# Performance work log

Hardware: AMD Instinct MI355X
Metric: run time of the kernel (lower is better)

The kernel has to match this reference:

```python
import jax, jax.numpy as jnp
import numpy as np

HIDDEN = 4096
NUM_EXPERTS = 64
TOPK = 2
N_TOKENS = 16384


def setup_inputs() -> dict:
    key = jax.random.key(0)
    k_x, k_w, k_b = jax.random.split(key, 3)
    x = jax.random.normal(k_x, (N_TOKENS, HIDDEN), dtype=jnp.float32)
    # torch.nn.Linear: weight [out, in], bias [out], uniform(-1/sqrt(in), 1/sqrt(in))
    bound = 1.0 / np.sqrt(HIDDEN)
    W = jax.random.uniform(k_w, (NUM_EXPERTS, HIDDEN), dtype=jnp.float32, minval=-bound, maxval=bound)
    b = jax.random.uniform(k_b, (NUM_EXPERTS,), dtype=jnp.float32, minval=-bound, maxval=bound)
    return {"x": x, "W": W, "b": b}


def reference(x, W, b):
    # logits: [N, E] = x @ W.T + b
    logits = jnp.einsum("nh,eh->ne", x, W) + b
    probs = jax.nn.softmax(logits, axis=1)
    # torch.topk along dim=1 returns (values, indices), sorted descending
    values, indices = jax.lax.top_k(probs, TOPK)
    return values, indices
```

## Files before the change

### kernel.cpp

```cpp
#include <hip/hip_runtime.h>
#include <hip/hip_bf16.h>
#include <math.h>

#define HIDDEN   4096
#define NEXP     64
#define NTOK     16384
#define KCHUNKS  8
#define KC       (HIDDEN / KCHUNKS)
#define BK       32
#define BT       64
#define LDSS     68

__global__ __launch_bounds__(64, 2)
void gemm_partial(const float* __restrict__ x, const float* __restrict__ W,
                  float* __restrict__ part) {
    __shared__ float Xs[BK][LDSS];
    __shared__ float Ws[BK][LDSS];

    const int tid  = threadIdx.x;
    const int tile = blockIdx.x;
    const int kc   = blockIdx.y;
    const int t0   = tile * BT;

    const int lrow = tid & 7;
    const int lcol = tid >> 3;
    const int i    = tid & 7;
    const int j    = tid >> 3;

    float acc[8][8];
#pragma unroll
    for (int m = 0; m < 8; ++m)
#pragma unroll
        for (int e = 0; e < 8; ++e) acc[m][e] = 0.f;

    for (int kb = 0; kb < KC / BK; ++kb) {
        const int kg = kc * KC + kb * BK + lrow * 4;
#pragma unroll
        for (int p = 0; p < 8; ++p) {
            const int r = p * 8 + lcol;
            const float4 xv = *(const float4*)&x[(size_t)(t0 + r) * HIDDEN + kg];
            Xs[lrow * 4 + 0][r] = xv.x;
            Xs[lrow * 4 + 1][r] = xv.y;
            Xs[lrow * 4 + 2][r] = xv.z;
            Xs[lrow * 4 + 3][r] = xv.w;
            const float4 wv = *(const float4*)&W[(size_t)r * HIDDEN + kg];
            Ws[lrow * 4 + 0][r] = wv.x;
            Ws[lrow * 4 + 1][r] = wv.y;
            Ws[lrow * 4 + 2][r] = wv.z;
            Ws[lrow * 4 + 3][r] = wv.w;
        }
        __syncthreads();
#pragma unroll
        for (int kk = 0; kk < BK; ++kk) {
            const float4 xa = *(const float4*)&Xs[kk][i * 8];
            const float4 xb = *(const float4*)&Xs[kk][i * 8 + 4];
            const float4 wa = *(const float4*)&Ws[kk][j * 8];
            const float4 wb = *(const float4*)&Ws[kk][j * 8 + 4];
            const float xr[8] = {xa.x, xa.y, xa.z, xa.w, xb.x, xb.y, xb.z, xb.w};
            const float wr[8] = {wa.x, wa.y, wa.z, wa.w, wb.x, wb.y, wb.z, wb.w};
#pragma unroll
            for (int m = 0; m < 8; ++m)
#pragma unroll
                for (int e = 0; e < 8; ++e)
                    acc[m][e] = fmaf(xr[m], wr[e], acc[m][e]);
        }
        __syncthreads();
    }

    float* dst = part + ((size_t)kc * NTOK + t0) * NEXP;
#pragma unroll
    for (int m = 0; m < 8; ++m) {
        const int tok = i * 8 + m;
#pragma unroll
        for (int h = 0; h < 2; ++h) {
            float4 o = make_float4(acc[m][h * 4 + 0], acc[m][h * 4 + 1],
                                   acc[m][h * 4 + 2], acc[m][h * 4 + 3]);
            *(float4*)&dst[(size_t)tok * NEXP + j * 8 + h * 4] = o;
        }
    }
}

__global__ __launch_bounds__(256)
void softmax_top2(const float* __restrict__ part, const float* __restrict__ bias,
                  float* __restrict__ out) {
    const int lane = threadIdx.x & 63;
    const int wid  = threadIdx.x >> 6;
    const int t    = blockIdx.x * 4 + wid;

    float l = bias[lane];
#pragma unroll
    for (int c = 0; c < KCHUNKS; ++c)
        l += part[((size_t)c * NTOK + t) * NEXP + lane];

    float m = l;
#pragma unroll
    for (int s = 32; s > 0; s >>= 1)
        m = fmaxf(m, __shfl_xor(m, s, 64));

    float ssum = expf(l - m);
#pragma unroll
    for (int s = 32; s > 0; s >>= 1)
        ssum += __shfl_xor(ssum, s, 64);

    float v1 = l; int i1 = lane;
#pragma unroll
    for (int s = 32; s > 0; s >>= 1) {
        float ov = __shfl_xor(v1, s, 64);
        int   oi = __shfl_xor(i1, s, 64);
        if (ov > v1 || (ov == v1 && oi < i1)) { v1 = ov; i1 = oi; }
    }
    float v2 = (lane == i1) ? -INFINITY : l;
    int   i2 = lane;
#pragma unroll
    for (int s = 32; s > 0; s >>= 1) {
        float ov = __shfl_xor(v2, s, 64);
        int   oi = __shfl_xor(i2, s, 64);
        if (ov > v2 || (ov == v2 && oi < i2)) { v2 = ov; i2 = oi; }
    }

    if (lane == 0) {
        const float inv = 1.0f / ssum;
        out[(size_t)t * 2 + 0] = inv;
        out[(size_t)t * 2 + 1] = expf(v2 - m) * inv;
        out[(size_t)2 * NTOK + t * 2 + 0] = (float)i1;
        out[(size_t)2 * NTOK + t * 2 + 1] = (float)i2;
    }
}

extern "C" void kernel_launch(void* const* d_in, const int* in_sizes, int n_in,
                              void* d_out, int out_size, void* d_ws, size_t ws_size,
                              hipStream_t stream) {
    const float* x  = (const float*)d_in[0];
    const float* W  = (const float*)d_in[1];
    const float* b  = (const float*)d_in[2];
    float* out  = (float*)d_out;
    float* part = (float*)d_ws;

    dim3 g1(NTOK / BT, KCHUNKS);
    gemm_partial<<<g1, 64, 0, stream>>>(x, W, part);
    softmax_top2<<<NTOK / 4, 256, 0, stream>>>(part, b, out);
}
```

Baseline: 399.7 us.

## Retile router GEMM to 256-thread blocks with register-prefetched global loads

The GEMM kernel moves from 64-thread blocks over 64 tokens to 256-thread blocks over 128 tokens. Each thread now computes an 8x4 micro-tile instead of 8x8. The next K-slice of x and W is loaded into registers while the current slice is computed, overlapping global latency with FMA work. Bigger blocks give more waves per CU and reuse each W tile across more tokens, at the cost of a lower FMA-to-LDS-read ratio per thread.

```diff
diff --git a/kernel.cpp b/kernel.cpp
--- a/kernel.cpp
+++ b/kernel.cpp
@@ -8,76 +8,92 @@
 #define KCHUNKS  8
 #define KC       (HIDDEN / KCHUNKS)
 #define BK       32
-#define BT       64
-#define LDSS     68
+#define BT       128
+#define XS       132
+#define WS       68
 
-__global__ __launch_bounds__(64, 2)
+__device__ __forceinline__ void fma4(float4& a, float s, const float4& v) {
+    a.x = fmaf(s, v.x, a.x);
+    a.y = fmaf(s, v.y, a.y);
+    a.z = fmaf(s, v.z, a.z);
+    a.w = fmaf(s, v.w, a.w);
+}
+
+__global__ __launch_bounds__(256, 4)
 void gemm_partial(const float* __restrict__ x, const float* __restrict__ W,
                   float* __restrict__ part) {
-    __shared__ float Xs[BK][LDSS];
-    __shared__ float Ws[BK][LDSS];
+    __shared__ float Xs[BK][XS];
+    __shared__ float Ws[BK][WS];
 
-    const int tid  = threadIdx.x;
-    const int tile = blockIdx.x;
-    const int kc   = blockIdx.y;
-    const int t0   = tile * BT;
+    const int tid = threadIdx.x;
+    const int t0  = blockIdx.x * BT;
+    const int kc  = blockIdx.y;
 
     const int lrow = tid & 7;
     const int lcol = tid >> 3;
-    const int i    = tid & 7;
-    const int j    = tid >> 3;
+    const int i = tid & 15;
+    const int j = tid >> 4;
 
-    float acc[8][8];
+    float4 acc4[8];
 #pragma unroll
-    for (int m = 0; m < 8; ++m)
-#pragma unroll
-        for (int e = 0; e < 8; ++e) acc[m][e] = 0.f;
+    for (int m = 0; m < 8; ++m) acc4[m] = make_float4(0.f, 0.f, 0.f, 0.f);
+
+    const int kbase = kc * KC;
+
+    float4 xp0, xp1, xp2, xp3, wp0, wp1;
+    {
+        const int kg = kbase + lrow * 4;
+        xp0 = *(const float4*)&x[(size_t)(t0 +  0 + lcol) * HIDDEN + kg];
+        xp1 = *(const float4*)&x[(size_t)(t0 + 32 + lcol) * HIDDEN + kg];
+        xp2 = *(const float4*)&x[(size_t)(t0 + 64 + lcol) * HIDDEN + kg];
+        xp3 = *(const float4*)&x[(size_t)(t0 + 96 + lcol) * HIDDEN + kg];
+        wp0 = *(const float4*)&W[(size_t)( 0 + lcol) * HIDDEN + kg];
+        wp1 = *(const float4*)&W[(size_t)(32 + lcol) * HIDDEN + kg];
+    }
 
     for (int kb = 0; kb < KC / BK; ++kb) {
-        const int kg = kc * KC + kb * BK + lrow * 4;
-#pragma unroll
-        for (int p = 0; p < 8; ++p) {
-            const int r = p * 8 + lcol;
-            const float4 xv = *(const float4*)&x[(size_t)(t0 + r) * HIDDEN + kg];
-            Xs[lrow * 4 + 0][r] = xv.x;
-            Xs[lrow * 4 + 1][r] = xv.y;
-            Xs[lrow * 4 + 2][r] = xv.z;
-            Xs[lrow * 4 + 3][r] = xv.w;
-            const float4 wv = *(const float4*)&W[(size_t)r * HIDDEN + kg];
-            Ws[lrow * 4 + 0][r] = wv.x;
-            Ws[lrow * 4 + 1][r] = wv.y;
-            Ws[lrow * 4 + 2][r] = wv.z;
-            Ws[lrow * 4 + 3][r] = wv.w;
+        const int kr = lrow * 4;
+        Xs[kr + 0][ 0 + lcol] = xp0.x; Xs[kr + 1][ 0 + lcol] = xp0.y;
+        Xs[kr + 2][ 0 + lcol] = xp0.z; Xs[kr + 3][ 0 + lcol] = xp0.w;
+        Xs[kr + 0][32 + lcol] = xp1.x; Xs[kr + 1][32 + lcol] = xp1.y;
+        Xs[kr + 2][32 + lcol] = xp1.z; Xs[kr + 3][32 + lcol] = xp1.w;
+        Xs[kr + 0][64 + lcol] = xp2.x; Xs[kr + 1][64 + lcol] = xp2.y;
+        Xs[kr + 2][64 + lcol] = xp2.z; Xs[kr + 3][64 + lcol] = xp2.w;
+        Xs[kr + 0][96 + lcol] = xp3.x; Xs[kr + 1][96 + lcol] = xp3.y;
+        Xs[kr + 2][96 + lcol] = xp3.z; Xs[kr + 3][96 + lcol] = xp3.w;
+        Ws[kr + 0][ 0 + lcol] = wp0.x; Ws[kr + 1][ 0 + lcol] = wp0.y;
+        Ws[kr + 2][ 0 + lcol] = wp0.z; Ws[kr + 3][ 0 + lcol] = wp0.w;
+        Ws[kr + 0][32 + lcol] = wp1.x; Ws[kr + 1][32 + lcol] = wp1.y;
+        Ws[kr + 2][32 + lcol] = wp1.z; Ws[kr + 3][32 + lcol] = wp1.w;
+        __syncthreads();
+
+        if (kb + 1 < KC / BK) {
+            const int kg = kbase + (kb + 1) * BK + lrow * 4;
+            xp0 = *(const float4*)&x[(size_t)(t0 +  0 + lcol) * HIDDEN + kg];
+            xp1 = *(const float4*)&x[(size_t)(t0 + 32 + lcol) * HIDDEN + kg];
+            xp2 = *(const float4*)&x[(size_t)(t0 + 64 + lcol) * HIDDEN + kg];
+            xp3 = *(const float4*)&x[(size_t)(t0 + 96 + lcol) * HIDDEN + kg];
+            wp0 = *(const float4*)&W[(size_t)( 0 + lcol) * HIDDEN + kg];
+            wp1 = *(const float4*)&W[(size_t)(32 + lcol) * HIDDEN + kg];
         }
-        __syncthreads();
+
 #pragma unroll
         for (int kk = 0; kk < BK; ++kk) {
             const float4 xa = *(const float4*)&Xs[kk][i * 8];
             const float4 xb = *(const float4*)&Xs[kk][i * 8 + 4];
-            const float4 wa = *(const float4*)&Ws[kk][j * 8];
-            const float4 wb = *(const float4*)&Ws[kk][j * 8 + 4];
-            const float xr[8] = {xa.x, xa.y, xa.z, xa.w, xb.x, xb.y, xb.z, xb.w};
-            const float wr[8] = {wa.x, wa.y, wa.z, wa.w, wb.x, wb.y, wb.z, wb.w};
-#pragma unroll
-            for (int m = 0; m < 8; ++m)
-#pragma unroll
-                for (int e = 0; e < 8; ++e)
-                    acc[m][e] = fmaf(xr[m], wr[e], acc[m][e]);
+            const float4 wv = *(const float4*)&Ws[kk][j * 4];
+            fma4(acc4[0], xa.x, wv); fma4(acc4[1], xa.y, wv);
+            fma4(acc4[2], xa.z, wv); fma4(acc4[3], xa.w, wv);
+            fma4(acc4[4], xb.x, wv); fma4(acc4[5], xb.y, wv);
+            fma4(acc4[6], xb.z, wv); fma4(acc4[7], xb.w, wv);
         }
         __syncthreads();
     }
 
-    float* dst = part + ((size_t)kc * NTOK + t0) * NEXP;
+    float* dst = part + ((size_t)kc * NTOK + t0 + i * 8) * NEXP + j * 4;
 #pragma unroll
-    for (int m = 0; m < 8; ++m) {
-        const int tok = i * 8 + m;
-#pragma unroll
-        for (int h = 0; h < 2; ++h) {
-            float4 o = make_float4(acc[m][h * 4 + 0], acc[m][h * 4 + 1],
-                                   acc[m][h * 4 + 2], acc[m][h * 4 + 3]);
-            *(float4*)&dst[(size_t)tok * NEXP + j * 8 + h * 4] = o;
-        }
-    }
+    for (int m = 0; m < 8; ++m)
+        *(float4*)&dst[(size_t)m * NEXP] = acc4[m];
 }
 
 __global__ __launch_bounds__(256)
@@ -137,6 +153,6 @@
     float* part = (float*)d_ws;
 
     dim3 g1(NTOK / BT, KCHUNKS);
-    gemm_partial<<<g1, 64, 0, stream>>>(x, W, part);
+    gemm_partial<<<g1, 256, 0, stream>>>(x, W, part);
     softmax_top2<<<NTOK / 4, 256, 0, stream>>>(part, b, out);
 }
```

Result: slower. 480.3 us (+20.1%).

## Enlarge GEMM token tile to 256 with XOR-swizzled shared memory layout

Applied to the files above, without the earlier changes.

The partial GEMM block grows from 64 threads covering 64 tokens to 256 threads covering 256 tokens, so each K-chunk loads W once per 256 tokens instead of once per 64. The padded shared arrays are replaced by XOR-swizzled layouts to avoid bank conflicts on the transposed stores and the vector reads. The per-thread micro-tile stays 8x8, now held as float4 accumulators. The larger block uses more shared memory and may lower occupancy, and the grid shrinks to 512 blocks.

```diff
diff --git a/kernel.cpp b/kernel.cpp
--- a/kernel.cpp
+++ b/kernel.cpp
@@ -8,75 +8,91 @@
 #define KCHUNKS  8
 #define KC       (HIDDEN / KCHUNKS)
 #define BK       32
-#define BT       64
-#define LDSS     68
+#define BT       256
 
-__global__ __launch_bounds__(64, 2)
+__device__ __forceinline__ void fma4(float4& a, float s, const float4& v) {
+    a.x = fmaf(s, v.x, a.x);
+    a.y = fmaf(s, v.y, a.y);
+    a.z = fmaf(s, v.z, a.z);
+    a.w = fmaf(s, v.w, a.w);
+}
+
+__global__ __launch_bounds__(256, 2)
 void gemm_partial(const float* __restrict__ x, const float* __restrict__ W,
                   float* __restrict__ part) {
-    __shared__ float Xs[BK][LDSS];
-    __shared__ float Ws[BK][LDSS];
+    __shared__ float Xs[BK * BT];
+    __shared__ float Ws[BK * NEXP];
 
     const int tid  = threadIdx.x;
-    const int tile = blockIdx.x;
+    const int t0   = blockIdx.x * BT;
     const int kc   = blockIdx.y;
-    const int t0   = tile * BT;
-
     const int lrow = tid & 7;
     const int lcol = tid >> 3;
-    const int i    = tid & 7;
-    const int j    = tid >> 3;
+    const int i    = tid & 31;
+    const int j    = tid >> 5;
 
-    float acc[8][8];
+    float4 acc[16];
 #pragma unroll
-    for (int m = 0; m < 8; ++m)
-#pragma unroll
-        for (int e = 0; e < 8; ++e) acc[m][e] = 0.f;
+    for (int m = 0; m < 16; ++m) acc[m] = make_float4(0.f, 0.f, 0.f, 0.f);
 
     for (int kb = 0; kb < KC / BK; ++kb) {
         const int kg = kc * KC + kb * BK + lrow * 4;
+
 #pragma unroll
-        for (int p = 0; p < 8; ++p) {
-            const int r = p * 8 + lcol;
-            const float4 xv = *(const float4*)&x[(size_t)(t0 + r) * HIDDEN + kg];
-            Xs[lrow * 4 + 0][r] = xv.x;
-            Xs[lrow * 4 + 1][r] = xv.y;
-            Xs[lrow * 4 + 2][r] = xv.z;
-            Xs[lrow * 4 + 3][r] = xv.w;
-            const float4 wv = *(const float4*)&W[(size_t)r * HIDDEN + kg];
-            Ws[lrow * 4 + 0][r] = wv.x;
-            Ws[lrow * 4 + 1][r] = wv.y;
-            Ws[lrow * 4 + 2][r] = wv.z;
-            Ws[lrow * 4 + 3][r] = wv.w;
+        for (int p = 0; p < 2; ++p) {
+            const int e  = lcol + p * 32;
+            const float4 wv = *(const float4*)&W[(size_t)e * HIDDEN + kg];
+            const int cw = ((((e >> 2) ^ lrow) << 2) + (e & 3));
+            Ws[(lrow * 4 + 0) * NEXP + cw] = wv.x;
+            Ws[(lrow * 4 + 1) * NEXP + cw] = wv.y;
+            Ws[(lrow * 4 + 2) * NEXP + cw] = wv.z;
+            Ws[(lrow * 4 + 3) * NEXP + cw] = wv.w;
+        }
+#pragma unroll
+        for (int s = 0; s < 8; ++s) {
+            const int t  = s * 32 + lcol;
+            const float4 xv = *(const float4*)&x[(size_t)(t0 + t) * HIDDEN + kg];
+            const int cx = ((((t >> 2) ^ lrow) << 2) + (t & 3));
+            Xs[(lrow * 4 + 0) * BT + cx] = xv.x;
+            Xs[(lrow * 4 + 1) * BT + cx] = xv.y;
+            Xs[(lrow * 4 + 2) * BT + cx] = xv.z;
+            Xs[(lrow * 4 + 3) * BT + cx] = xv.w;
         }
         __syncthreads();
+
 #pragma unroll
-        for (int kk = 0; kk < BK; ++kk) {
-            const float4 xa = *(const float4*)&Xs[kk][i * 8];
-            const float4 xb = *(const float4*)&Xs[kk][i * 8 + 4];
-            const float4 wa = *(const float4*)&Ws[kk][j * 8];
-            const float4 wb = *(const float4*)&Ws[kk][j * 8 + 4];
-            const float xr[8] = {xa.x, xa.y, xa.z, xa.w, xb.x, xb.y, xb.z, xb.w};
-            const float wr[8] = {wa.x, wa.y, wa.z, wa.w, wb.x, wb.y, wb.z, wb.w};
+        for (int g = 0; g < 8; ++g) {
+            const int xo = ((i ^ g) << 2);
+            const int wo = ((j ^ g) << 2);
 #pragma unroll
-            for (int m = 0; m < 8; ++m)
-#pragma unroll
-                for (int e = 0; e < 8; ++e)
-                    acc[m][e] = fmaf(xr[m], wr[e], acc[m][e]);
+            for (int q = 0; q < 4; ++q) {
+                const int kk = (g << 2) + q;
+                const float4 xa = *(const float4*)&Xs[kk * BT + xo];
+                const float4 xb = *(const float4*)&Xs[kk * BT + xo + 128];
+                const float4 wa = *(const float4*)&Ws[kk * NEXP + wo];
+                const float4 wb = *(const float4*)&Ws[kk * NEXP + wo + 32];
+                fma4(acc[0],  xa.x, wa); fma4(acc[1],  xa.x, wb);
+                fma4(acc[2],  xa.y, wa); fma4(acc[3],  xa.y, wb);
+                fma4(acc[4],  xa.z, wa); fma4(acc[5],  xa.z, wb);
+                fma4(acc[6],  xa.w, wa); fma4(acc[7],  xa.w, wb);
+                fma4(acc[8],  xb.x, wa); fma4(acc[9],  xb.x, wb);
+                fma4(acc[10], xb.y, wa); fma4(acc[11], xb.y, wb);
+                fma4(acc[12], xb.z, wa); fma4(acc[13], xb.z, wb);
+                fma4(acc[14], xb.w, wa); fma4(acc[15], xb.w, wb);
+            }
         }
         __syncthreads();
     }
 
-    float* dst = part + ((size_t)kc * NTOK + t0) * NEXP;
+    const size_t obase = ((size_t)kc * NTOK + t0) * NEXP;
 #pragma unroll
-    for (int m = 0; m < 8; ++m) {
-        const int tok = i * 8 + m;
-#pragma unroll
-        for (int h = 0; h < 2; ++h) {
-            float4 o = make_float4(acc[m][h * 4 + 0], acc[m][h * 4 + 1],
-                                   acc[m][h * 4 + 2], acc[m][h * 4 + 3]);
-            *(float4*)&dst[(size_t)tok * NEXP + j * 8 + h * 4] = o;
-        }
+    for (int m = 0; m < 4; ++m) {
+        float* r0 = part + obase + (size_t)(i * 4 + m) * NEXP;
+        float* r1 = part + obase + (size_t)(i * 4 + m + 128) * NEXP;
+        *(float4*)&r0[j * 4]      = acc[m * 2 + 0];
+        *(float4*)&r0[j * 4 + 32] = acc[m * 2 + 1];
+        *(float4*)&r1[j * 4]      = acc[8 + m * 2 + 0];
+        *(float4*)&r1[j * 4 + 32] = acc[8 + m * 2 + 1];
     }
 }
 
@@ -137,6 +153,6 @@
     float* part = (float*)d_ws;
 
     dim3 g1(NTOK / BT, KCHUNKS);
-    gemm_partial<<<g1, 64, 0, stream>>>(x, W, part);
+    gemm_partial<<<g1, 256, 0, stream>>>(x, W, part);
     softmax_top2<<<NTOK / 4, 256, 0, stream>>>(part, b, out);
 }
```

Result: slower. 460.4 us (+15.2%).
